# Kernel tuning notes

Measured on AMD Instinct MI355X. Metric: run time of the kernel, lower is better.

The kernel has to match this reference:

```python
import jax, jax.numpy as jnp
import numpy as np

B, T, C, H, U = 16, 2048, 512, 4, 250
L, R = 1, 1              # l_order, r_order -> depthwise kernel size 3
K = L + R + 1
SMOOTH, NOISE = 1.0, 0.0  # smooth_factor, noise_threshold


def setup_inputs() -> dict:
    key = jax.random.key(0)
    k0, k1, k2, k3 = jax.random.split(key, 4)
    hidden = jax.random.normal(k0, (B, T, C), dtype=jnp.float32)
    mask = jnp.ones((B, 1, T), dtype=jnp.float32)
    target_label_length = jax.random.randint(k1, (B,), 0, U).astype(jnp.int32)
    # parameters
    conv_w = jax.random.normal(k2, (C, 1, K), dtype=jnp.float32) / np.sqrt(K)   # depthwise Conv1d weight [O, I/g=1, K]
    conv_b = jnp.zeros((C,), dtype=jnp.float32)
    lin_w = jax.random.normal(k3, (1, C), dtype=jnp.float32) / np.sqrt(C)       # cif_output Linear(idim, 1)
    lin_b = jnp.zeros((1,), dtype=jnp.float32)
    sigma = jnp.full((H,), 0.5, dtype=jnp.float32)
    sigma_bias = jnp.zeros((H,), dtype=jnp.float32)
    return {
        "hidden": hidden, "mask": mask, "target_label_length": target_label_length,
        "max_token": U, "conv_w": conv_w, "conv_b": conv_b,
        "lin_w": lin_w, "lin_b": lin_b, "sigma": sigma, "sigma_bias": sigma_bias,
    }


def reference(hidden, mask, target_label_length, max_token, conv_w, conv_b, lin_w, lin_b, sigma, sigma_bias):
    b, t, c = hidden.shape
    h = sigma.shape[0]
    # --- alpha prediction branch ---
    context = jnp.swapaxes(hidden, 1, 2)                       # [B, C, T]
    queries = jnp.pad(context, ((0, 0), (0, 0), (L, R)))       # ConstantPad1d((l, r), 0)
    memory = jax.lax.conv_general_dilated(
        queries, conv_w, window_strides=(1,), padding='VALID',
        feature_group_count=c, dimension_numbers=('NCH', 'OIH', 'NCH'))
    memory = memory + conv_b[None, :, None]
    out = jnp.swapaxes(memory + context, 1, 2)                 # [B, T, C]  (dropout = identity in eval)
    out = jax.nn.relu(out)
    out = out @ lin_w.T + lin_b                                # [B, T, 1]
    alphas = jax.nn.relu(jax.nn.sigmoid(out) * SMOOTH - NOISE)
    mask_bt1 = jnp.swapaxes(mask, -1, -2)                      # [B, T, 1]
    alphas = (alphas * mask_bt1)[..., 0]                       # [B, T]
    mask_bt = mask_bt1[..., 0]                                 # [B, T]
    # --- CIF scaling to target length ---
    target_length = target_label_length.astype(jnp.float32)   # [B]
    token_num = alphas.sum(-1)                                 # [B] (pre-scaling, as in torch)
    alphas = alphas * (target_length / token_num)[:, None]
    alignment = jnp.cumsum(alphas, axis=-1)                    # [B, T]
    # --- Gaussian soft-segment attention ---
    fire_positions = jnp.arange(max_token, dtype=alphas.dtype) + 0.5            # [U]
    dist = fire_positions[None, None, :, None] - alignment[:, None, None, :]    # [B, 1, U, T]
    scores = -(dist * sigma[None, :, None, None]) ** 2 + sigma_bias[None, :, None, None]  # [B, H, U, T]
    scores = jnp.where(mask_bt[:, None, None, :] > 0, scores, -jnp.inf)
    weights = jax.nn.softmax(scores, axis=-1)                  # [B, H, U, T]
    n_hidden = hidden.reshape(b, t, h, c // h).transpose(0, 2, 1, 3)            # [B, H, T, Dh]
    acoustic = jnp.einsum('bhut,bhtd->bhud', weights, n_hidden)                 # [B, H, U, Dh]
    acoustic_embeds = acoustic.transpose(0, 2, 1, 3).reshape(b, max_token, c)   # [B, U, C]
    return acoustic_embeds, token_num, alphas
```

## Files before the change

kernel.cpp:

```cpp
#include <hip/hip_runtime.h>
#include <hip/hip_bf16.h>

namespace {
constexpr int kB = 16, kT = 2048, kC = 512, kH = 4, kU = 250, kDH = 128;
constexpr int kDS = 4;
constexpr int kDW = 32;
constexpr int kTT = 256;
constexpr int kNST = kT / kTT;
constexpr int kPitch = 264;
}

typedef __attribute__((ext_vector_type(8))) short short8;
typedef __attribute__((ext_vector_type(4))) float float4v;

__device__ __forceinline__ short f2bf(float x) {
    union { float f; unsigned int u; } v; v.f = x;
    unsigned int r = (v.u + 0x7FFFu + ((v.u >> 16) & 1u)) >> 16;
    return (short)r;
}

__global__ __launch_bounds__(256) void k1_alpha(
    const float* __restrict__ hid, const float* __restrict__ mask,
    const float* __restrict__ conv_w, const float* __restrict__ conv_b,
    const float* __restrict__ lin_w, const float* __restrict__ lin_b,
    float* __restrict__ alpha_raw)
{
    const int wave = threadIdx.x >> 6, lane = threadIdx.x & 63;
    const int gw = blockIdx.x * 4 + wave;
    const int b = gw >> 8;
    const int t0 = (gw & 255) << 3;
    const int c0 = lane * 8;

    float cw[24], cb[8], lw[8];
    #pragma unroll
    for (int i = 0; i < 6; i++) *(float4*)&cw[i*4] = ((const float4*)(conv_w + c0*3))[i];
    *(float4*)&cb[0] = *(const float4*)(conv_b + c0);
    *(float4*)&cb[4] = *(const float4*)(conv_b + c0 + 4);
    *(float4*)&lw[0] = *(const float4*)(lin_w + c0);
    *(float4*)&lw[4] = *(const float4*)(lin_w + c0 + 4);
    const float lb = lin_b[0];

    float r[10][8];
    const float* base = hid + ((size_t)b * kT + t0) * kC + c0;
    #pragma unroll
    for (int i = 0; i < 10; i++) {
        const int tt = t0 + i - 1;
        if (tt >= 0 && tt < kT) {
            const float* p = base + (ptrdiff_t)(i - 1) * kC;
            *(float4*)&r[i][0] = *(const float4*)p;
            *(float4*)&r[i][4] = *(const float4*)(p + 4);
        } else {
            #pragma unroll
            for (int j = 0; j < 8; j++) r[i][j] = 0.f;
        }
    }

    float sums[8];
    #pragma unroll
    for (int j = 0; j < 8; j++) {
        float acc = 0.f;
        #pragma unroll
        for (int k = 0; k < 8; k++) {
            float m = fmaf(r[j][k], cw[k*3],
                      fmaf(r[j+1][k], cw[k*3+1],
                      fmaf(r[j+2][k], cw[k*3+2], cb[k])));
            float v = m + r[j+1][k];
            v = v > 0.f ? v : 0.f;
            acc = fmaf(v, lw[k], acc);
        }
        #pragma unroll
        for (int off = 32; off >= 1; off >>= 1) acc += __shfl_xor(acc, off, 64);
        sums[j] = acc;
    }
    if (lane == 0) {
        #pragma unroll
        for (int j = 0; j < 8; j++) {
            float s = sums[j] + lb;
            float a = 1.f / (1.f + expf(-s));
            alpha_raw[(size_t)b * kT + t0 + j] = a * mask[(size_t)b * kT + t0 + j];
        }
    }
}

__global__ __launch_bounds__(256) void k2_scan(
    const float* __restrict__ alpha_raw, const float* __restrict__ mask,
    const int* __restrict__ target,
    float* __restrict__ align_out,
    float* __restrict__ out_tok, float* __restrict__ out_alpha)
{
    __shared__ float wtot[4];
    __shared__ float s_tot;
    const int b = blockIdx.x;
    const int tid = threadIdx.x;
    const int wave = tid >> 6, lane = tid & 63;

    const float* ar = alpha_raw + (size_t)b * kT + tid * 8;
    float raw[8], pre[8];
    float s = 0.f;
    #pragma unroll
    for (int j = 0; j < 8; j++) { raw[j] = ar[j]; s += raw[j]; pre[j] = s; }

    float sc = s;
    #pragma unroll
    for (int off = 1; off <= 32; off <<= 1) {
        float v = __shfl_up(sc, off, 64);
        sc = (lane >= off) ? sc + v : sc;
    }
    if (lane == 63) wtot[wave] = sc;
    __syncthreads();
    if (tid == 0) {
        float a0 = wtot[0], a1 = wtot[1], a2 = wtot[2], a3 = wtot[3];
        wtot[0] = 0.f; wtot[1] = a0; wtot[2] = a0 + a1; wtot[3] = a0 + a1 + a2;
        s_tot = a0 + a1 + a2 + a3;
    }
    __syncthreads();
    const float run = s_tot;
    const float scale = (run != 0.f) ? ((float)target[b] / run) : 0.f;
    const float basev = wtot[wave] + (sc - s);
    if (tid == 0) out_tok[b] = run;

    const float* mp = mask + (size_t)b * kT + tid * 8;
    float* al = align_out + (size_t)b * kT + tid * 8;
    float* oa = out_alpha + (size_t)b * kT + tid * 8;
    #pragma unroll
    for (int j = 0; j < 8; j++) {
        float cum = (basev + pre[j]) * scale;
        al[j] = (mp[j] > 0.f) ? cum : 1.0e30f;
        oa[j] = raw[j] * scale;
    }
}

__global__ __launch_bounds__(1024) void k3_attn(
    const float* __restrict__ hid, const float* __restrict__ align_m,
    const float* __restrict__ sigma, float* __restrict__ out_ac)
{
    __shared__ float al_s[kT];
    __shared__ unsigned short bT[kDW * kPitch];

    const int ds = blockIdx.x, h = blockIdx.y, b = blockIdx.z;
    const int tid = threadIdx.x;
    const int wave = tid >> 6, lane = tid & 63;
    const int lm = lane & 15, quad = lane >> 4;
    const float sig = sigma[h];

    if (tid < 512)
        ((float4*)al_s)[tid] = ((const float4*)(align_m + (size_t)b * kT))[tid];
    __syncthreads();

    const int u_base = wave * 16;
    const float du = (float)(u_base + lm) + 0.5f;
    const float dusig = du * sig;
    int pos = 0;
    #pragma unroll
    for (int stp = 1024; stp >= 1; stp >>= 1) {
        int np = pos + stp;
        pos = (al_s[np - 1] < du) ? np : pos;
    }
    float d1 = (pos < kT) ? al_s[pos] - du : 3.0e30f;
    float d0 = (pos > 0) ? du - al_s[pos - 1] : 3.0e30f;
    float dmin = fminf(fminf(d0, d1), 300.f);
    float ms = dmin * sig;
    const float mu_pos = ms * ms;

    float dmax_l = dmin;
    #pragma unroll
    for (int off = 32; off >= 1; off >>= 1) dmax_l = fmaxf(dmax_l, __shfl_xor(dmax_l, off, 64));
    const float W = (sig > 1e-6f) ? 9.4f / sig : 3.0e30f;
    const float lo_b = (float)u_base + 0.5f - dmax_l - W;
    const float hi_b = (float)u_base + 15.5f + dmax_l + W;
    int p_lo = 0, p_hi = 0;
    #pragma unroll
    for (int stp = 1024; stp >= 1; stp >>= 1) {
        int n1 = p_lo + stp; p_lo = (al_s[n1 - 1] < lo_b) ? n1 : p_lo;
        int n2 = p_hi + stp; p_hi = (al_s[n2 - 1] < hi_b) ? n2 : p_hi;
    }
    const int ks_lo = p_lo >> 5;
    const int ks_end = (p_hi + 31) >> 5;

    float4v acc0 = (float4v)(0.f), acc1 = (float4v)(0.f);
    float lsum = 0.f;

    const int tl = (tid & 127) * 2;
    const int dbase = (tid >> 7) * 4;
    const float* hrow = hid + (size_t)b * kT * kC + h * kDH + ds * kDW + dbase;

    float4 a0, a1;
    a0 = *(const float4*)(hrow + (size_t)tl * kC);
    a1 = *(const float4*)(hrow + (size_t)(tl + 1) * kC);

    for (int st = 0; st < kNST; st++) {
        __syncthreads();
        {
            const float* p0 = (const float*)&a0;
            const float* p1 = (const float*)&a1;
            #pragma unroll
            for (int e = 0; e < 4; e++) {
                unsigned int lo = (unsigned int)(unsigned short)f2bf(p0[e]);
                unsigned int hi = (unsigned int)(unsigned short)f2bf(p1[e]);
                *(unsigned int*)&bT[(dbase + e) * kPitch + tl] = lo | (hi << 16);
            }
        }
        __syncthreads();
        if (st + 1 < kNST) {
            const float* p0 = hrow + (size_t)((st + 1) * kTT + tl) * kC;
            a0 = *(const float4*)p0;
            a1 = *(const float4*)(p0 + kC);
        }

        #pragma unroll
        for (int ks = 0; ks < 8; ks++) {
            const int kg = st * 8 + ks;
            if (kg < ks_lo || kg >= ks_end) continue;
            const int kb = kg * 32;

            float alv[8];
            *(float4*)&alv[0] = *(const float4*)&al_s[kb + quad * 8];
            *(float4*)&alv[4] = *(const float4*)&al_s[kb + quad * 8 + 4];

            short8 afrag;
            #pragma unroll
            for (int j = 0; j < 8; j++) {
                float d = fmaf(-alv[j], sig, dusig);
                float e = __expf(fmaf(-d, d, mu_pos));
                lsum += e;
                afrag[j] = f2bf(e);
            }
            short8 bf0 = *(const short8*)&bT[lm * kPitch + ks * 32 + quad * 8];
            short8 bf1 = *(const short8*)&bT[(16 + lm) * kPitch + ks * 32 + quad * 8];
            acc0 = __builtin_amdgcn_mfma_f32_16x16x32_bf16(afrag, bf0, acc0, 0, 0, 0);
            acc1 = __builtin_amdgcn_mfma_f32_16x16x32_bf16(afrag, bf1, acc1, 0, 0, 0);
        }
    }

    float lv = lsum;
    lv += __shfl_xor(lv, 16, 64);
    lv += __shfl_xor(lv, 32, 64);
    #pragma unroll
    for (int r = 0; r < 4; r++) {
        const int ur = quad * 4 + r;
        float rl = __shfl(lv, ur, 64);
        float linv = (rl > 1e-30f) ? 1.f / rl : 0.f;
        const int u = u_base + ur;
        if (u < kU) {
            float* dst = out_ac + ((size_t)(b * kU + u)) * kC + h * kDH + ds * kDW + lm;
            dst[0]  = acc0[r] * linv;
            dst[16] = acc1[r] * linv;
        }
    }
}

extern "C" void kernel_launch(void* const* d_in, const int* in_sizes, int n_in,
                              void* d_out, int out_size, void* d_ws, size_t ws_size,
                              hipStream_t stream) {
    const float* hid    = (const float*)d_in[0];
    const float* mask   = (const float*)d_in[1];
    const int*   tgt    = (const int*)d_in[2];
    const float* conv_w = (const float*)d_in[4];
    const float* conv_b = (const float*)d_in[5];
    const float* lin_w  = (const float*)d_in[6];
    const float* lin_b  = (const float*)d_in[7];
    const float* sigma  = (const float*)d_in[8];

    float* alpha_raw = (float*)d_ws;
    float* align_m   = alpha_raw + (size_t)kB * kT;

    float* out_ac    = (float*)d_out;
    float* out_tok   = out_ac + (size_t)kB * kU * kC;
    float* out_alpha = out_tok + kB;

    k1_alpha<<<kB * kT / 32, 256, 0, stream>>>(hid, mask, conv_w, conv_b, lin_w, lin_b, alpha_raw);
    k2_scan<<<kB, 256, 0, stream>>>(alpha_raw, mask, tgt, align_m, out_tok, out_alpha);
    k3_attn<<<dim3(kDS, kH, kB), 1024, 0, stream>>>(hid, align_m, sigma, out_ac);
}
```

Before: 138.0 us.

## Fuse scan into attention kernel, split tokens across blocks, skip inactive time tiles

Removes the separate scan kernel: each attention block now recomputes the cumulative alignment of its batch row in shared memory, and one block per batch writes token_num and the scaled alphas. The attention grid is doubled with 512-thread blocks that each cover half the output tokens. A block-wide union of the Gaussian support window is computed so whole 256-step time tiles with no contribution are skipped, avoiding their hidden-state loads. The window bound is changed to a quadratic-distance criterion. In exchange the scan work is repeated in every block and the register prefetch of the next tile is dropped, so load latency is no longer overlapped with compute.

Result: slower. 146.7 us (+6.3%).

```diff
diff --git a/kernel.cpp b/kernel.cpp
--- a/kernel.cpp
+++ b/kernel.cpp
@@ -1,5 +1,6 @@
 #include <hip/hip_runtime.h>
 #include <hip/hip_bf16.h>
+#include <math.h>
 
 namespace {
 constexpr int kB = 16, kT = 2048, kC = 512, kH = 4, kU = 250, kDH = 128;
@@ -82,72 +83,68 @@
     }
 }
 
-__global__ __launch_bounds__(256) void k2_scan(
-    const float* __restrict__ alpha_raw, const float* __restrict__ mask,
-    const int* __restrict__ target,
-    float* __restrict__ align_out,
-    float* __restrict__ out_tok, float* __restrict__ out_alpha)
-{
-    __shared__ float wtot[4];
-    __shared__ float s_tot;
-    const int b = blockIdx.x;
-    const int tid = threadIdx.x;
-    const int wave = tid >> 6, lane = tid & 63;
-
-    const float* ar = alpha_raw + (size_t)b * kT + tid * 8;
-    float raw[8], pre[8];
-    float s = 0.f;
-    #pragma unroll
-    for (int j = 0; j < 8; j++) { raw[j] = ar[j]; s += raw[j]; pre[j] = s; }
-
-    float sc = s;
-    #pragma unroll
-    for (int off = 1; off <= 32; off <<= 1) {
-        float v = __shfl_up(sc, off, 64);
-        sc = (lane >= off) ? sc + v : sc;
-    }
-    if (lane == 63) wtot[wave] = sc;
-    __syncthreads();
-    if (tid == 0) {
-        float a0 = wtot[0], a1 = wtot[1], a2 = wtot[2], a3 = wtot[3];
-        wtot[0] = 0.f; wtot[1] = a0; wtot[2] = a0 + a1; wtot[3] = a0 + a1 + a2;
-        s_tot = a0 + a1 + a2 + a3;
-    }
-    __syncthreads();
-    const float run = s_tot;
-    const float scale = (run != 0.f) ? ((float)target[b] / run) : 0.f;
-    const float basev = wtot[wave] + (sc - s);
-    if (tid == 0) out_tok[b] = run;
-
-    const float* mp = mask + (size_t)b * kT + tid * 8;
-    float* al = align_out + (size_t)b * kT + tid * 8;
-    float* oa = out_alpha + (size_t)b * kT + tid * 8;
-    #pragma unroll
-    for (int j = 0; j < 8; j++) {
-        float cum = (basev + pre[j]) * scale;
-        al[j] = (mp[j] > 0.f) ? cum : 1.0e30f;
-        oa[j] = raw[j] * scale;
-    }
-}
-
-__global__ __launch_bounds__(1024) void k3_attn(
-    const float* __restrict__ hid, const float* __restrict__ align_m,
-    const float* __restrict__ sigma, float* __restrict__ out_ac)
+__global__ __launch_bounds__(512) void k3_attn(
+    const float* __restrict__ hid, const float* __restrict__ alpha_raw,
+    const float* __restrict__ mask, const int* __restrict__ target,
+    const float* __restrict__ sigma,
+    float* __restrict__ out_ac, float* __restrict__ out_tok, float* __restrict__ out_alpha)
 {
     __shared__ float al_s[kT];
     __shared__ unsigned short bT[kDW * kPitch];
-
-    const int ds = blockIdx.x, h = blockIdx.y, b = blockIdx.z;
+    __shared__ float woff[8];
+    __shared__ float s_tot;
+    __shared__ int wlo[8], whi[8];
+    __shared__ int s_blo, s_bhi;
+
+    const int u2 = blockIdx.x & 1, ds = blockIdx.x >> 1;
+    const int h = blockIdx.y, b = blockIdx.z;
     const int tid = threadIdx.x;
     const int wave = tid >> 6, lane = tid & 63;
     const int lm = lane & 15, quad = lane >> 4;
     const float sig = sigma[h];
 
-    if (tid < 512)
-        ((float4*)al_s)[tid] = ((const float4*)(align_m + (size_t)b * kT))[tid];
-    __syncthreads();
-
-    const int u_base = wave * 16;
+    float4 av = ((const float4*)(alpha_raw + (size_t)b * kT))[tid];
+    float pre[4];
+    pre[0] = av.x; pre[1] = pre[0] + av.y; pre[2] = pre[1] + av.z; pre[3] = pre[2] + av.w;
+    const float s = pre[3];
+    float sc = s;
+    #pragma unroll
+    for (int off = 1; off <= 32; off <<= 1) {
+        float v = __shfl_up(sc, off, 64);
+        sc = (lane >= off) ? sc + v : sc;
+    }
+    if (lane == 63) woff[wave] = sc;
+    __syncthreads();
+    if (tid == 0) {
+        float run = 0.f;
+        #pragma unroll
+        for (int w = 0; w < 8; w++) { float x = woff[w]; woff[w] = run; run += x; }
+        s_tot = run;
+    }
+    __syncthreads();
+    const float tot = s_tot;
+    const float scale = (tot != 0.f) ? ((float)target[b] / tot) : 0.f;
+    const float basev = woff[wave] + (sc - s);
+    float4 mv = ((const float4*)(mask + (size_t)b * kT))[tid];
+    {
+        float alv[4];
+        const float* mp = (const float*)&mv;
+        #pragma unroll
+        for (int j = 0; j < 4; j++) {
+            float cum = (basev + pre[j]) * scale;
+            alv[j] = (mp[j] > 0.f) ? cum : 1.0e30f;
+        }
+        *(float4*)&al_s[tid * 4] = *(float4*)&alv[0];
+    }
+    if (blockIdx.x == 0 && h == 0) {
+        if (tid == 0) out_tok[b] = tot;
+        float4 oa;
+        oa.x = av.x * scale; oa.y = av.y * scale; oa.z = av.z * scale; oa.w = av.w * scale;
+        ((float4*)(out_alpha + (size_t)b * kT))[tid] = oa;
+    }
+    __syncthreads();
+
+    const int u_base = u2 * 128 + wave * 16;
     const float du = (float)(u_base + lm) + 0.5f;
     const float dusig = du * sig;
     int pos = 0;
@@ -158,16 +155,17 @@
     }
     float d1 = (pos < kT) ? al_s[pos] - du : 3.0e30f;
     float d0 = (pos > 0) ? du - al_s[pos - 1] : 3.0e30f;
-    float dmin = fminf(fminf(d0, d1), 300.f);
-    float ms = dmin * sig;
+    float dmin = fminf(d0, d1);
+    float ms = fminf(dmin, 1.0e4f) * sig;
     const float mu_pos = ms * ms;
 
     float dmax_l = dmin;
     #pragma unroll
-    for (int off = 32; off >= 1; off >>= 1) dmax_l = fmaxf(dmax_l, __shfl_xor(dmax_l, off, 64));
-    const float W = (sig > 1e-6f) ? 9.4f / sig : 3.0e30f;
-    const float lo_b = (float)u_base + 0.5f - dmax_l - W;
-    const float hi_b = (float)u_base + 15.5f + dmax_l + W;
+    for (int off = 8; off >= 1; off >>= 1) dmax_l = fmaxf(dmax_l, __shfl_xor(dmax_l, off, 64));
+    const float c21 = (sig > 1e-3f) ? 21.0f / (sig * sig) : 9.0e60f;
+    const float bound = sqrtf(fmaf(dmax_l, dmax_l, c21));
+    const float lo_b = (float)u_base + 0.5f - bound;
+    const float hi_b = (float)u_base + 15.5f + bound;
     int p_lo = 0, p_hi = 0;
     #pragma unroll
     for (int stp = 1024; stp >= 1; stp >>= 1) {
@@ -176,36 +174,51 @@
     }
     const int ks_lo = p_lo >> 5;
     const int ks_end = (p_hi + 31) >> 5;
+    if (lane == 0) { wlo[wave] = p_lo; whi[wave] = p_hi; }
+    __syncthreads();
+    if (tid == 0) {
+        int lo = kT, hi = 0;
+        #pragma unroll
+        for (int w = 0; w < 8; w++) { lo = min(lo, wlo[w]); hi = max(hi, whi[w]); }
+        s_blo = lo; s_bhi = hi;
+    }
+    __syncthreads();
+    const int blk_lo = s_blo, blk_hi = s_bhi;
 
     float4v acc0 = (float4v)(0.f), acc1 = (float4v)(0.f);
     float lsum = 0.f;
 
     const int tl = (tid & 127) * 2;
-    const int dbase = (tid >> 7) * 4;
+    const int dbase = (tid >> 7) * 8;
     const float* hrow = hid + (size_t)b * kT * kC + h * kDH + ds * kDW + dbase;
 
-    float4 a0, a1;
-    a0 = *(const float4*)(hrow + (size_t)tl * kC);
-    a1 = *(const float4*)(hrow + (size_t)(tl + 1) * kC);
-
     for (int st = 0; st < kNST; st++) {
+        const int t_lo = st * kTT;
+        if (t_lo + kTT <= blk_lo || t_lo >= blk_hi) continue;
         __syncthreads();
         {
+            const float* src = hrow + (size_t)(t_lo + tl) * kC;
+            float4 a0 = *(const float4*)src;
+            float4 a1 = *(const float4*)(src + 4);
+            float4 b0 = *(const float4*)(src + kC);
+            float4 b1 = *(const float4*)(src + kC + 4);
             const float* p0 = (const float*)&a0;
-            const float* p1 = (const float*)&a1;
+            const float* p1 = (const float*)&b0;
             #pragma unroll
             for (int e = 0; e < 4; e++) {
                 unsigned int lo = (unsigned int)(unsigned short)f2bf(p0[e]);
                 unsigned int hi = (unsigned int)(unsigned short)f2bf(p1[e]);
                 *(unsigned int*)&bT[(dbase + e) * kPitch + tl] = lo | (hi << 16);
             }
+            p0 = (const float*)&a1; p1 = (const float*)&b1;
+            #pragma unroll
+            for (int e = 0; e < 4; e++) {
+                unsigned int lo = (unsigned int)(unsigned short)f2bf(p0[e]);
+                unsigned int hi = (unsigned int)(unsigned short)f2bf(p1[e]);
+                *(unsigned int*)&bT[(dbase + 4 + e) * kPitch + tl] = lo | (hi << 16);
+            }
         }
         __syncthreads();
-        if (st + 1 < kNST) {
-            const float* p0 = hrow + (size_t)((st + 1) * kTT + tl) * kC;
-            a0 = *(const float4*)p0;
-            a1 = *(const float4*)(p0 + kC);
-        }
 
         #pragma unroll
         for (int ks = 0; ks < 8; ks++) {
@@ -262,13 +275,12 @@
     const float* sigma  = (const float*)d_in[8];
 
     float* alpha_raw = (float*)d_ws;
-    float* align_m   = alpha_raw + (size_t)kB * kT;
 
     float* out_ac    = (float*)d_out;
     float* out_tok   = out_ac + (size_t)kB * kU * kC;
     float* out_alpha = out_tok + kB;
 
     k1_alpha<<<kB * kT / 32, 256, 0, stream>>>(hid, mask, conv_w, conv_b, lin_w, lin_b, alpha_raw);
-    k2_scan<<<kB, 256, 0, stream>>>(alpha_raw, mask, tgt, align_m, out_tok, out_alpha);
-    k3_attn<<<dim3(kDS, kH, kB), 1024, 0, stream>>>(hid, align_m, sigma, out_ac);
-}
+    k3_attn<<<dim3(2 * kDS, kH, kB), 512, 0, stream>>>(hid, alpha_raw, mask, tgt, sigma,
+                                                       out_ac, out_tok, out_alpha);
+}
```
